# Optimization experiments

Hardware: AMD Instinct MI355X
Metric: run time of the kernel (lower is better)

The kernel has to match this reference:

```python
import jax, jax.numpy as jnp
import numpy as np

C = 1.0            # curvature
N = 50000          # nodes
E = 800000         # edges (avg degree 16)
D_IN = 127         # raw feature dim (+1 time col -> 128)
D = 128            # hidden dim
N_CLS = 40         # classes
EPS = 1e-8


def setup_inputs() -> dict:
    key = jax.random.key(0)
    ks = jax.random.split(key, 8)
    stdv = 1.0 / np.sqrt(D)
    node_feat = jax.random.normal(ks[0], (N, D_IN), jnp.float32)
    W1 = jax.random.uniform(ks[1], (D, D), jnp.float32, -stdv, stdv)
    W2 = jax.random.uniform(ks[2], (D, D), jnp.float32, -stdv, stdv)
    b1 = jnp.zeros((D,), jnp.float32)
    b2 = jnp.zeros((D,), jnp.float32)
    s1 = jnp.asarray(np.log(10.0), jnp.float32)
    s2 = jnp.asarray(np.log(10.0), jnp.float32)
    # class prototypes: random points on the hyperboloid <p,p>_L = -C
    cls_space = jax.random.normal(ks[3], (N_CLS, D - 1), jnp.float32) * stdv
    cls_time = jnp.sqrt(C + jnp.sum(cls_space * cls_space, -1, keepdims=True))
    cls = jnp.concatenate([cls_time, cls_space], axis=-1)
    cls_bias = jnp.zeros((N_CLS,), jnp.float32)
    edge_w = jax.random.uniform(ks[4], (E,), jnp.float32)
    edge_row = jax.random.randint(ks[5], (E,), 0, N, jnp.int32)
    edge_col = jax.random.randint(ks[6], (E,), 0, N, jnp.int32)
    return dict(node_feat=node_feat, W1=W1, b1=b1, s1=s1, W2=W2, b2=b2, s2=s2,
                cls=cls, cls_bias=cls_bias, edge_w=edge_w,
                edge_row=edge_row, edge_col=edge_col)


def _expmap0(u):
    # u: [N, D-1] spatial tangent at origin; lift to hyperboloid (k = C)
    sc = jnp.sqrt(C)
    nrm = jnp.clip(jnp.linalg.norm(u, axis=-1, keepdims=True), EPS)
    time = sc * jnp.cosh(nrm / sc)
    space = sc * jnp.sinh(nrm / sc) * (u / nrm)
    return jnp.concatenate([time, space], axis=-1)


def _lorentz_linear(x, W, b, log_s, nonlin):
    if nonlin:
        x = jax.nn.relu(x)
    x = x @ W.T + b                                   # [N, D]
    xn = x[:, 1:]                                     # spatial part
    time = jax.nn.sigmoid(x[:, :1]) * jnp.minimum(jnp.exp(log_s), 10.0) \
           + (jnp.sqrt(C) + 0.5)
    sq = jnp.clip(jnp.sum(xn * xn, -1, keepdims=True), EPS)
    scale = (time * time - C) / sq
    return jnp.concatenate([time, xn * jnp.sqrt(jnp.clip(scale, EPS))], axis=-1)


def _lorentz_agg(x, edge_w, edge_row, edge_col):
    # spmm: support[i] = sum_{(i,j) in E} w_ij * x[j]
    msg = x[edge_col] * edge_w[:, None]               # [E, D]
    s = jax.ops.segment_sum(msg, edge_row, num_segments=N)
    # -<s,s>_L = s0^2 - sum_{i>0} si^2
    neg_inner = s[:, :1] * s[:, :1] - jnp.sum(s[:, 1:] * s[:, 1:], -1, keepdims=True)
    denom = jnp.sqrt(jnp.clip(jnp.abs(neg_inner), EPS)) / jnp.sqrt(C)
    return s / denom


def reference(node_feat, W1, b1, s1, W2, b2, s2, cls, cls_bias,
              edge_w, edge_row, edge_col):
    x = _expmap0(node_feat)                           # [N, 128] on hyperboloid
    # layer 1 (no nonlin)
    x = _lorentz_linear(x, W1, b1, s1, nonlin=False)
    x = _lorentz_agg(x, edge_w, edge_row, edge_col)
    # layer 2 (relu)
    x = _lorentz_linear(x, W2, b2, s2, nonlin=True)
    x = _lorentz_agg(x, edge_w, edge_row, edge_col)
    # Lorentz decoder: 2c + 2*cinner(x, cls) + bias
    x_signed = jnp.concatenate([-x[:, :1], x[:, 1:]], axis=-1)
    logits = 2.0 * C + 2.0 * (x_signed @ cls.T) + cls_bias
    return logits
```

## Files before the change

kernel.cpp:

```cpp
#include <hip/hip_runtime.h>
#include <hip/hip_fp16.h>
#include <math.h>

#define NN 50000
#define DD 128
#define NCLS 40
#define EPSV 1e-8f
#define ELLCAP 64

typedef unsigned int uint4n __attribute__((ext_vector_type(4)));

__device__ __forceinline__ float waveReduceSum(float v) {
    for (int off = 32; off > 0; off >>= 1) v += __shfl_xor(v, off, 64);
    return v;
}

__device__ __forceinline__ float bcastlane0(float v) {
    return __int_as_float(__builtin_amdgcn_readfirstlane(__float_as_int(v)));
}

__device__ __forceinline__ float h_lo(unsigned int w) {
    return __half2float(__ushort_as_half((unsigned short)(w & 0xffffu)));
}
__device__ __forceinline__ float h_hi(unsigned int w) {
    return __half2float(__ushort_as_half((unsigned short)(w >> 16)));
}
__device__ __forceinline__ unsigned int h_pack(float a, float b) {
    return (unsigned int)__half_as_ushort(__float2half(a)) |
           ((unsigned int)__half_as_ushort(__float2half(b)) << 16);
}
__device__ __forceinline__ float fexp(float x) {
    return __builtin_amdgcn_exp2f(x * 1.44269504089f);
}
__device__ __forceinline__ float frcp(float x) { return __builtin_amdgcn_rcpf(x); }
__device__ __forceinline__ float frsq(float x) { return __builtin_amdgcn_rsqf(x); }


__global__ void fill_ell_kernel(const int* __restrict__ erow, const int* __restrict__ ecol,
                                const float* __restrict__ ew, int* __restrict__ cnt,
                                unsigned int* __restrict__ ell, int E) {
    for (int e = blockIdx.x * blockDim.x + threadIdx.x; e < E; e += gridDim.x * blockDim.x) {
        int r = erow[e];
        int p = atomicAdd(&cnt[r], 1);
        if (p < ELLCAP) {
            unsigned int packed = (unsigned int)ecol[e] |
                ((unsigned int)__half_as_ushort(__float2half(ew[e])) << 16);
            ell[(long)r * ELLCAP + p] = packed;
        }
    }
}

__global__ void packwt_kernel(const float* __restrict__ W1, unsigned int* __restrict__ p1,
                              const float* __restrict__ W2, unsigned int* __restrict__ p2) {
    int b = blockIdx.x;
    const float* W = (b < 32) ? W1 : W2;
    unsigned int* P = (b < 32) ? p1 : p2;
    int a = (b & 31) * 256 + threadIdx.x;
    int pr = a >> 7;
    int rem = a & 127;
    int l = rem >> 1, kl = rem & 1;
    int k = 2 * pr + kl;
    P[a] = h_pack(W[(2 * l) * 128 + k], W[(2 * l + 1) * 128 + k]);
}

#define RPW 8
__global__ __launch_bounds__(512, 4) void linear1_kernel(
    const float* __restrict__ X, const unsigned int* __restrict__ Wp,
    const float* __restrict__ bias, const float* __restrict__ logs,
    unsigned int* __restrict__ outh, int n)
{
    __shared__ unsigned int wS[8192];
    __shared__ float xrow[8][RPW * 128];
    int tid = threadIdx.x;
    int wid = tid >> 6, lane = tid & 63;
    #pragma unroll
    for (int i = 0; i < 4; ++i) {
        int idx = tid * 4 + i * 2048;
        *(uint4n*)(wS + idx) = *(const uint4n*)(Wp + idx);
    }
    __syncthreads();
    float2 bv = *(const float2*)(bias + 2 * lane);
    float sval = fminf(fexp(logs[0]), 10.f);
    float* xbase = xrow[wid];
    int nslabs = n / RPW;
    for (int slab = blockIdx.x * 8 + wid; slab < nslabs; slab += gridDim.x * 8) {
        int row0 = slab * RPW;
        #pragma unroll
        for (int r = 0; r < RPW; ++r) {
            int row = row0 + r;
            const float* src = X + (long)row * 127;
            float u0 = src[2 * lane];
            float u1 = (2 * lane + 1 < 127) ? src[2 * lane + 1] : 0.f;
            float ss = waveReduceSum(u0 * u0 + u1 * u1);
            float nrm = fmaxf(sqrtf(ss), EPSV);
            float ex = fexp(nrm), exn = fexp(-nrm);
            float ch = 0.5f * (ex + exn);
            float coef = 0.5f * (ex - exn) * frcp(nrm);
            if (lane == 0) xbase[r * 128] = ch;
            xbase[r * 128 + 1 + 2 * lane] = coef * u0;
            if (2 * lane + 1 < 127) xbase[r * 128 + 2 + 2 * lane] = coef * u1;
        }
        float2 acc[RPW];
        #pragma unroll
        for (int r = 0; r < RPW; ++r) acc[r] = make_float2(0.f, 0.f);
        #pragma unroll 4
        for (int k0 = 0; k0 < 128; k0 += 4) {
            uint2 wa = *(const uint2*)(wS + (k0 >> 1) * 128 + 2 * lane);
            uint2 wb = *(const uint2*)(wS + (k0 >> 1) * 128 + 128 + 2 * lane);
            float2 w0 = make_float2(h_lo(wa.x), h_hi(wa.x));
            float2 w1 = make_float2(h_lo(wa.y), h_hi(wa.y));
            float2 w2 = make_float2(h_lo(wb.x), h_hi(wb.x));
            float2 w3 = make_float2(h_lo(wb.y), h_hi(wb.y));
            #pragma unroll
            for (int r = 0; r < RPW; ++r) {
                float4 xq = *(const float4*)(xbase + r * 128 + k0);
                acc[r].x = fmaf(xq.x, w0.x, acc[r].x);
                acc[r].y = fmaf(xq.x, w0.y, acc[r].y);
                acc[r].x = fmaf(xq.y, w1.x, acc[r].x);
                acc[r].y = fmaf(xq.y, w1.y, acc[r].y);
                acc[r].x = fmaf(xq.z, w2.x, acc[r].x);
                acc[r].y = fmaf(xq.z, w2.y, acc[r].y);
                acc[r].x = fmaf(xq.w, w3.x, acc[r].x);
                acc[r].y = fmaf(xq.w, w3.y, acc[r].y);
            }
        }
        #pragma unroll
        for (int r = 0; r < RPW; ++r) {
            float ax = acc[r].x + bv.x;
            float ay = acc[r].y + bv.y;
            float t0 = __shfl(ax, 0, 64);
            float ssq = waveReduceSum(ax * ax + ay * ay);
            float timev = sval * frcp(1.f + fexp(-t0)) + 1.5f;
            float sq = fmaxf(ssq - t0 * t0, EPSV);
            float fac = sqrtf(fmaxf((timev * timev - 1.f) * frcp(sq), EPSV));
            float o0 = (lane == 0) ? timev : ax * fac;
            __builtin_nontemporal_store(h_pack(o0, ay * fac),
                                        &outh[(long)(row0 + r) * 64 + lane]);
        }
    }
}

__global__ __launch_bounds__(512, 4) void linear2_kernel(
    const unsigned int* __restrict__ Xh, const unsigned int* __restrict__ Wp,
    const float* __restrict__ bias, const float* __restrict__ logs,
    unsigned int* __restrict__ outh, int n)
{
    __shared__ unsigned int wS[8192];
    __shared__ float xrow[8][RPW * 128];
    int tid = threadIdx.x;
    int wid = tid >> 6, lane = tid & 63;
    #pragma unroll
    for (int i = 0; i < 4; ++i) {
        int idx = tid * 4 + i * 2048;
        *(uint4n*)(wS + idx) = *(const uint4n*)(Wp + idx);
    }
    __syncthreads();
    float2 bv = *(const float2*)(bias + 2 * lane);
    float sval = fminf(fexp(logs[0]), 10.f);
    float* xbase = xrow[wid];
    int nslabs = n / RPW;
    for (int slab = blockIdx.x * 8 + wid; slab < nslabs; slab += gridDim.x * 8) {
        int row0 = slab * RPW;
        #pragma unroll
        for (int r = 0; r < RPW; ++r) {
            unsigned int u = __builtin_nontemporal_load(&Xh[(long)(row0 + r) * 64 + lane]);
            *(float2*)(xbase + r * 128 + 2 * lane) = make_float2(h_lo(u), h_hi(u));
        }
        float2 acc[RPW];
        #pragma unroll
        for (int r = 0; r < RPW; ++r) acc[r] = make_float2(0.f, 0.f);
        #pragma unroll 4
        for (int k0 = 0; k0 < 128; k0 += 4) {
            uint2 wa = *(const uint2*)(wS + (k0 >> 1) * 128 + 2 * lane);
            uint2 wb = *(const uint2*)(wS + (k0 >> 1) * 128 + 128 + 2 * lane);
            float2 w0 = make_float2(h_lo(wa.x), h_hi(wa.x));
            float2 w1 = make_float2(h_lo(wa.y), h_hi(wa.y));
            float2 w2 = make_float2(h_lo(wb.x), h_hi(wb.x));
            float2 w3 = make_float2(h_lo(wb.y), h_hi(wb.y));
            #pragma unroll
            for (int r = 0; r < RPW; ++r) {
                float4 xq = *(const float4*)(xbase + r * 128 + k0);
                acc[r].x = fmaf(xq.x, w0.x, acc[r].x);
                acc[r].y = fmaf(xq.x, w0.y, acc[r].y);
                acc[r].x = fmaf(xq.y, w1.x, acc[r].x);
                acc[r].y = fmaf(xq.y, w1.y, acc[r].y);
                acc[r].x = fmaf(xq.z, w2.x, acc[r].x);
                acc[r].y = fmaf(xq.z, w2.y, acc[r].y);
                acc[r].x = fmaf(xq.w, w3.x, acc[r].x);
                acc[r].y = fmaf(xq.w, w3.y, acc[r].y);
            }
        }
        #pragma unroll
        for (int r = 0; r < RPW; ++r) {
            float ax = acc[r].x + bv.x;
            float ay = acc[r].y + bv.y;
            float t0 = __shfl(ax, 0, 64);
            float ssq = waveReduceSum(ax * ax + ay * ay);
            float timev = sval * frcp(1.f + fexp(-t0)) + 1.5f;
            float sq = fmaxf(ssq - t0 * t0, EPSV);
            float fac = sqrtf(fmaxf((timev * timev - 1.f) * frcp(sq), EPSV));
            float o0 = (lane == 0) ? timev : ax * fac;
            __builtin_nontemporal_store(h_pack(o0, ay * fac),
                                        &outh[(long)(row0 + r) * 64 + lane]);
        }
    }
}


#define GATHER_BODY(accs, eptr, idx)                                       \
    {                                                                      \
        unsigned int cw = eptr[idx];                                       \
        float w = h_hi(cw);                                                \
        uint4 xw = *(const uint4*)(Xh + (long)(cw & 0xffffu) * 64 + l16 * 4); \
        accs[0] = fmaf(w, h_lo(xw.x), accs[0]);                            \
        accs[1] = fmaf(w, h_hi(xw.x), accs[1]);                            \
        accs[2] = fmaf(w, h_lo(xw.y), accs[2]);                            \
        accs[3] = fmaf(w, h_hi(xw.y), accs[3]);                            \
        accs[4] = fmaf(w, h_lo(xw.z), accs[4]);                            \
        accs[5] = fmaf(w, h_hi(xw.z), accs[5]);                            \
        accs[6] = fmaf(w, h_lo(xw.w), accs[6]);                            \
        accs[7] = fmaf(w, h_hi(xw.w), accs[7]);                            \
    }

#define REDUCE8(accs)                                                      \
    _Pragma("unroll")                                                      \
    for (int q = 0; q < 8; ++q) {                                          \
        accs[q] += __shfl_xor(accs[q], 16, 64);                            \
        accs[q] += __shfl_xor(accs[q], 32, 64);                            \
    }

#define GATHER_PAIR()                                                      \
    int rowA = 2 * pair, rowB = rowA + 1;                                  \
    int cA = min(cnt[rowA], ELLCAP), cB = min(cnt[rowB], ELLCAP);          \
    const unsigned int* eA = ell + (long)rowA * ELLCAP;                    \
    const unsigned int* eB = ell + (long)rowB * ELLCAP;                    \
    float aA[8] = {0,0,0,0,0,0,0,0};                                       \
    float aB[8] = {0,0,0,0,0,0,0,0};                                       \
    {                                                                      \
        int ia = g, ib = g;                                                \
        while (ia < cA && ib < cB) {                                       \
            GATHER_BODY(aA, eA, ia)                                        \
            GATHER_BODY(aB, eB, ib)                                        \
            ia += 4; ib += 4;                                              \
        }                                                                  \
        while (ia < cA) { GATHER_BODY(aA, eA, ia) ia += 4; }               \
        while (ib < cB) { GATHER_BODY(aB, eB, ib) ib += 4; }               \
    }                                                                      \
    REDUCE8(aA)                                                            \
    REDUCE8(aB)

#define SS16(ss)                                                           \
    ss += __shfl_xor(ss, 1, 64); ss += __shfl_xor(ss, 2, 64);              \
    ss += __shfl_xor(ss, 4, 64); ss += __shfl_xor(ss, 8, 64);

__global__ __launch_bounds__(256, 8) void gather_norm_kernel(
    const unsigned int* __restrict__ Xh, const int* __restrict__ cnt,
    const unsigned int* __restrict__ ell, unsigned int* __restrict__ outh, int n)
{
    int wid = threadIdx.x >> 6, lane = threadIdx.x & 63;
    int g = lane >> 4, l16 = lane & 15;
    int npairs = n >> 1;
    for (int pair = blockIdx.x * 4 + wid; pair < npairs; pair += gridDim.x * 4) {
        GATHER_PAIR()
        float ssA = aA[0]*aA[0]+aA[1]*aA[1]+aA[2]*aA[2]+aA[3]*aA[3]
                  + aA[4]*aA[4]+aA[5]*aA[5]+aA[6]*aA[6]+aA[7]*aA[7];
        float ssB = aB[0]*aB[0]+aB[1]*aB[1]+aB[2]*aB[2]+aB[3]*aB[3]
                  + aB[4]*aB[4]+aB[5]*aB[5]+aB[6]*aB[6]+aB[7]*aB[7];
        SS16(ssA)
        SS16(ssB)
        float t0A = bcastlane0(aA[0]);
        float t0B = bcastlane0(aB[0]);
        float invA = frsq(fmaxf(fabsf(2.f * t0A * t0A - ssA), EPSV));
        float invB = frsq(fmaxf(fabsf(2.f * t0B * t0B - ssB), EPSV));
        if (g == 0) {
            uint4n o;
            o.x = h_pack(fmaxf(aA[0]*invA,0.f), fmaxf(aA[1]*invA,0.f));
            o.y = h_pack(fmaxf(aA[2]*invA,0.f), fmaxf(aA[3]*invA,0.f));
            o.z = h_pack(fmaxf(aA[4]*invA,0.f), fmaxf(aA[5]*invA,0.f));
            o.w = h_pack(fmaxf(aA[6]*invA,0.f), fmaxf(aA[7]*invA,0.f));
            __builtin_nontemporal_store(o, (uint4n*)(outh + (long)rowA * 64 + l16 * 4));
        } else if (g == 1) {
            uint4n o;
            o.x = h_pack(fmaxf(aB[0]*invB,0.f), fmaxf(aB[1]*invB,0.f));
            o.y = h_pack(fmaxf(aB[2]*invB,0.f), fmaxf(aB[3]*invB,0.f));
            o.z = h_pack(fmaxf(aB[4]*invB,0.f), fmaxf(aB[5]*invB,0.f));
            o.w = h_pack(fmaxf(aB[6]*invB,0.f), fmaxf(aB[7]*invB,0.f));
            __builtin_nontemporal_store(o, (uint4n*)(outh + (long)rowB * 64 + l16 * 4));
        }
    }
}

__global__ __launch_bounds__(256, 8) void gather_logits_kernel(
    const unsigned int* __restrict__ Xh, const int* __restrict__ cnt,
    const unsigned int* __restrict__ ell,
    const float* __restrict__ cls, const float* __restrict__ cbias,
    float* __restrict__ outp, int n)
{
    __shared__ unsigned int clsP[NCLS * 66];
    __shared__ float cbS[NCLS];
    __shared__ float xsrow[4][2][128];
    int tid = threadIdx.x;
    for (int idx = tid; idx < NCLS * 64; idx += 256) {
        int c = idx >> 6, kk = idx & 63;
        clsP[c * 66 + kk] = h_pack(cls[c * 128 + 2 * kk], cls[c * 128 + 2 * kk + 1]);
    }
    if (tid < NCLS) cbS[tid] = cbias[tid];
    __syncthreads();
    int wid = tid >> 6, lane = tid & 63;
    int g = lane >> 4, l16 = lane & 15;
    float* xsA = xsrow[wid][0];
    float* xsB = xsrow[wid][1];
    int npairs = n >> 1;
    for (int pair = blockIdx.x * 4 + wid; pair < npairs; pair += gridDim.x * 4) {
        GATHER_PAIR()
        float ssA = aA[0]*aA[0]+aA[1]*aA[1]+aA[2]*aA[2]+aA[3]*aA[3]
                  + aA[4]*aA[4]+aA[5]*aA[5]+aA[6]*aA[6]+aA[7]*aA[7];
        float ssB = aB[0]*aB[0]+aB[1]*aB[1]+aB[2]*aB[2]+aB[3]*aB[3]
                  + aB[4]*aB[4]+aB[5]*aB[5]+aB[6]*aB[6]+aB[7]*aB[7];
        SS16(ssA)
        SS16(ssB)
        float t0A = bcastlane0(aA[0]);
        float t0B = bcastlane0(aB[0]);
        float invA = frsq(fmaxf(fabsf(2.f * t0A * t0A - ssA), EPSV));
        float invB = frsq(fmaxf(fabsf(2.f * t0B * t0B - ssB), EPSV));
        if (g == 0) {
            float v0 = aA[0] * invA;
            if (l16 == 0) v0 = -v0;
            float* xp = xsA + l16 * 8;
            *(float4*)xp       = make_float4(v0, aA[1]*invA, aA[2]*invA, aA[3]*invA);
            *(float4*)(xp + 4) = make_float4(aA[4]*invA, aA[5]*invA, aA[6]*invA, aA[7]*invA);
        } else if (g == 1) {
            float v0 = aB[0] * invB;
            if (l16 == 0) v0 = -v0;
            float* xp = xsB + l16 * 8;
            *(float4*)xp       = make_float4(v0, aB[1]*invB, aB[2]*invB, aB[3]*invB);
            *(float4*)(xp + 4) = make_float4(aB[4]*invB, aB[5]*invB, aB[6]*invB, aB[7]*invB);
        }
        if (lane < NCLS) {
            float dA = 0.f, dB = 0.f;
            const unsigned int* cp = clsP + lane * 66;
            #pragma unroll 8
            for (int kk = 0; kk < 64; ++kk) {
                unsigned int u = cp[kk];
                float c0 = h_lo(u), c1 = h_hi(u);
                float2 xa = *(const float2*)(xsA + 2 * kk);
                float2 xb = *(const float2*)(xsB + 2 * kk);
                dA = fmaf(c0, xa.x, dA); dA = fmaf(c1, xa.y, dA);
                dB = fmaf(c0, xb.x, dB); dB = fmaf(c1, xb.y, dB);
            }
            outp[(long)rowA * NCLS + lane] = 2.f + 2.f * dA + cbS[lane];
            outp[(long)rowB * NCLS + lane] = 2.f + 2.f * dB + cbS[lane];
        }
    }
}


extern "C" void kernel_launch(void* const* d_in, const int* in_sizes, int n_in,
                              void* d_out, int out_size, void* d_ws, size_t ws_size,
                              hipStream_t stream) {
    const float* node_feat = (const float*)d_in[0];
    const float* W1   = (const float*)d_in[1];
    const float* b1   = (const float*)d_in[2];
    const float* s1   = (const float*)d_in[3];
    const float* W2   = (const float*)d_in[4];
    const float* b2   = (const float*)d_in[5];
    const float* s2   = (const float*)d_in[6];
    const float* cls  = (const float*)d_in[7];
    const float* cb   = (const float*)d_in[8];
    const float* ew   = (const float*)d_in[9];
    const int*   erow = (const int*)d_in[10];
    const int*   ecol = (const int*)d_in[11];
    float* outp = (float*)d_out;

    const int n = NN;
    const int E = in_sizes[9];

    unsigned int* bufH1 = (unsigned int*)d_ws;
    unsigned int* bufH2 = bufH1 + (size_t)NN * 64;
    int*   cnt    = (int*)(bufH2 + (size_t)NN * 64);
    unsigned int* ell = (unsigned int*)(cnt + NN);
    unsigned int* wp1 = ell + (size_t)NN * ELLCAP;
    unsigned int* wp2 = wp1 + 128 * 64;

    (void)hipMemsetAsync(cnt, 0, (size_t)NN * sizeof(int), stream);
    packwt_kernel<<<64, 256, 0, stream>>>(W1, wp1, W2, wp2);
    fill_ell_kernel<<<2048, 256, 0, stream>>>(erow, ecol, ew, cnt, ell, E);

    const int LGRID = (n / RPW + 7) / 8;
    const int PGRID = ((n >> 1) + 3) / 4;

    linear1_kernel<<<LGRID, 512, 0, stream>>>(node_feat, wp1, b1, s1, bufH1, n);
    gather_norm_kernel<<<PGRID, 256, 0, stream>>>(bufH1, cnt, ell, bufH2, n);
    linear2_kernel<<<LGRID, 512, 0, stream>>>(bufH2, wp2, b2, s2, bufH1, n);
    gather_logits_kernel<<<PGRID, 256, 0, stream>>>(bufH1, cnt, ell, cls, cb, outp, n);
}
```

Measured before the change: 230.2 us.

## Use packed fp16 dot2 instructions in linear kernels with half-precision shared rows

Both Lorentz linear kernels now keep activation rows in shared memory as packed fp16 pairs and compute the matmul with v_dot2 fp16 instructions. This replaces the per-element half-to-float conversions and scalar FMAs, and the weight packing layout is changed to pair consecutive k values. In linear1, the expmap output is divided by cosh before packing to fp16 to avoid overflow, and the accumulator is rescaled by cosh afterwards. This halves shared memory traffic for the activations and roughly halves ALU instructions, at the cost of fp16 rounding on the activations.

```diff
diff --git a/kernel.cpp b/kernel.cpp
--- a/kernel.cpp
+++ b/kernel.cpp
@@ -9,6 +9,28 @@
 #define ELLCAP 64
 
 typedef unsigned int uint4n __attribute__((ext_vector_type(4)));
+typedef _Float16 h2 __attribute__((ext_vector_type(2)));
+
+__device__ __forceinline__ float h_lo(unsigned int w) {
+    return __half2float(__ushort_as_half((unsigned short)(w & 0xffffu)));
+}
+__device__ __forceinline__ float h_hi(unsigned int w) {
+    return __half2float(__ushort_as_half((unsigned short)(w >> 16)));
+}
+
+__device__ __forceinline__ h2 as_h2(unsigned int u) {
+    union { unsigned int i; h2 h; } c; c.i = u; return c.h;
+}
+
+#if __has_builtin(__builtin_amdgcn_fdot2)
+#define FDOT2(xu, wu, acc) acc = __builtin_amdgcn_fdot2(as_h2(xu), as_h2(wu), acc, false);
+#else
+#define FDOT2(xu, wu, acc)                                                  \
+    {                                                                       \
+        acc = fmaf(h_lo(xu), h_lo(wu), acc);                                \
+        acc = fmaf(h_hi(xu), h_hi(wu), acc);                                \
+    }
+#endif
 
 __device__ __forceinline__ float waveReduceSum(float v) {
     for (int off = 32; off > 0; off >>= 1) v += __shfl_xor(v, off, 64);
@@ -19,12 +41,6 @@
     return __int_as_float(__builtin_amdgcn_readfirstlane(__float_as_int(v)));
 }
 
-__device__ __forceinline__ float h_lo(unsigned int w) {
-    return __half2float(__ushort_as_half((unsigned short)(w & 0xffffu)));
-}
-__device__ __forceinline__ float h_hi(unsigned int w) {
-    return __half2float(__ushort_as_half((unsigned short)(w >> 16)));
-}
 __device__ __forceinline__ unsigned int h_pack(float a, float b) {
     return (unsigned int)__half_as_ushort(__float2half(a)) |
            ((unsigned int)__half_as_ushort(__float2half(b)) << 16);
@@ -56,11 +72,8 @@
     const float* W = (b < 32) ? W1 : W2;
     unsigned int* P = (b < 32) ? p1 : p2;
     int a = (b & 31) * 256 + threadIdx.x;
-    int pr = a >> 7;
-    int rem = a & 127;
-    int l = rem >> 1, kl = rem & 1;
-    int k = 2 * pr + kl;
-    P[a] = h_pack(W[(2 * l) * 128 + k], W[(2 * l + 1) * 128 + k]);
+    int kk = a >> 7, col = a & 127;
+    P[a] = h_pack(W[col * 128 + 2 * kk], W[col * 128 + 2 * kk + 1]);
 }
 
 #define RPW 8
@@ -70,7 +83,7 @@
     unsigned int* __restrict__ outh, int n)
 {
     __shared__ unsigned int wS[8192];
-    __shared__ float xrow[8][RPW * 128];
+    __shared__ unsigned int xS[8][RPW * 64];
     int tid = threadIdx.x;
     int wid = tid >> 6, lane = tid & 63;
     #pragma unroll
@@ -81,10 +94,11 @@
     __syncthreads();
     float2 bv = *(const float2*)(bias + 2 * lane);
     float sval = fminf(fexp(logs[0]), 10.f);
-    float* xbase = xrow[wid];
+    unsigned int* xbase = xS[wid];
     int nslabs = n / RPW;
     for (int slab = blockIdx.x * 8 + wid; slab < nslabs; slab += gridDim.x * 8) {
         int row0 = slab * RPW;
+        float chv[RPW];
         #pragma unroll
         for (int r = 0; r < RPW; ++r) {
             int row = row0 + r;
@@ -96,38 +110,34 @@
             float ex = fexp(nrm), exn = fexp(-nrm);
             float ch = 0.5f * (ex + exn);
             float coef = 0.5f * (ex - exn) * frcp(nrm);
-            if (lane == 0) xbase[r * 128] = ch;
-            xbase[r * 128 + 1 + 2 * lane] = coef * u0;
-            if (2 * lane + 1 < 127) xbase[r * 128 + 2 + 2 * lane] = coef * u1;
+            chv[r] = ch;
+            float inv_ch = frcp(ch);
+            float u1p = __shfl(u1, (lane + 63) & 63, 64);
+            float xa = (lane == 0) ? 1.f : coef * u1p * inv_ch;
+            xbase[r * 64 + lane] = h_pack(xa, coef * u0 * inv_ch);
         }
         float2 acc[RPW];
         #pragma unroll
         for (int r = 0; r < RPW; ++r) acc[r] = make_float2(0.f, 0.f);
         #pragma unroll 4
-        for (int k0 = 0; k0 < 128; k0 += 4) {
-            uint2 wa = *(const uint2*)(wS + (k0 >> 1) * 128 + 2 * lane);
-            uint2 wb = *(const uint2*)(wS + (k0 >> 1) * 128 + 128 + 2 * lane);
-            float2 w0 = make_float2(h_lo(wa.x), h_hi(wa.x));
-            float2 w1 = make_float2(h_lo(wa.y), h_hi(wa.y));
-            float2 w2 = make_float2(h_lo(wb.x), h_hi(wb.x));
-            float2 w3 = make_float2(h_lo(wb.y), h_hi(wb.y));
+        for (int kk0 = 0; kk0 < 64; kk0 += 4) {
+            uint2 wp0 = *(const uint2*)(wS + (kk0 + 0) * 128 + 2 * lane);
+            uint2 wp1 = *(const uint2*)(wS + (kk0 + 1) * 128 + 2 * lane);
+            uint2 wp2 = *(const uint2*)(wS + (kk0 + 2) * 128 + 2 * lane);
+            uint2 wp3 = *(const uint2*)(wS + (kk0 + 3) * 128 + 2 * lane);
             #pragma unroll
             for (int r = 0; r < RPW; ++r) {
-                float4 xq = *(const float4*)(xbase + r * 128 + k0);
-                acc[r].x = fmaf(xq.x, w0.x, acc[r].x);
-                acc[r].y = fmaf(xq.x, w0.y, acc[r].y);
-                acc[r].x = fmaf(xq.y, w1.x, acc[r].x);
-                acc[r].y = fmaf(xq.y, w1.y, acc[r].y);
-                acc[r].x = fmaf(xq.z, w2.x, acc[r].x);
-                acc[r].y = fmaf(xq.z, w2.y, acc[r].y);
-                acc[r].x = fmaf(xq.w, w3.x, acc[r].x);
-                acc[r].y = fmaf(xq.w, w3.y, acc[r].y);
+                uint4 xq = *(const uint4*)(xbase + r * 64 + kk0);
+                FDOT2(xq.x, wp0.x, acc[r].x) FDOT2(xq.x, wp0.y, acc[r].y)
+                FDOT2(xq.y, wp1.x, acc[r].x) FDOT2(xq.y, wp1.y, acc[r].y)
+                FDOT2(xq.z, wp2.x, acc[r].x) FDOT2(xq.z, wp2.y, acc[r].y)
+                FDOT2(xq.w, wp3.x, acc[r].x) FDOT2(xq.w, wp3.y, acc[r].y)
             }
         }
         #pragma unroll
         for (int r = 0; r < RPW; ++r) {
-            float ax = acc[r].x + bv.x;
-            float ay = acc[r].y + bv.y;
+            float ax = acc[r].x * chv[r] + bv.x;
+            float ay = acc[r].y * chv[r] + bv.y;
             float t0 = __shfl(ax, 0, 64);
             float ssq = waveReduceSum(ax * ax + ay * ay);
             float timev = sval * frcp(1.f + fexp(-t0)) + 1.5f;
@@ -146,7 +156,7 @@
     unsigned int* __restrict__ outh, int n)
 {
     __shared__ unsigned int wS[8192];
-    __shared__ float xrow[8][RPW * 128];
+    __shared__ unsigned int xS[8][RPW * 64];
     int tid = threadIdx.x;
     int wid = tid >> 6, lane = tid & 63;
     #pragma unroll
@@ -157,37 +167,30 @@
     __syncthreads();
     float2 bv = *(const float2*)(bias + 2 * lane);
     float sval = fminf(fexp(logs[0]), 10.f);
-    float* xbase = xrow[wid];
+    unsigned int* xbase = xS[wid];
     int nslabs = n / RPW;
     for (int slab = blockIdx.x * 8 + wid; slab < nslabs; slab += gridDim.x * 8) {
         int row0 = slab * RPW;
         #pragma unroll
-        for (int r = 0; r < RPW; ++r) {
-            unsigned int u = __builtin_nontemporal_load(&Xh[(long)(row0 + r) * 64 + lane]);
-            *(float2*)(xbase + r * 128 + 2 * lane) = make_float2(h_lo(u), h_hi(u));
-        }
+        for (int r = 0; r < RPW; ++r)
+            xbase[r * 64 + lane] =
+                __builtin_nontemporal_load(&Xh[(long)(row0 + r) * 64 + lane]);
         float2 acc[RPW];
         #pragma unroll
         for (int r = 0; r < RPW; ++r) acc[r] = make_float2(0.f, 0.f);
         #pragma unroll 4
-        for (int k0 = 0; k0 < 128; k0 += 4) {
-            uint2 wa = *(const uint2*)(wS + (k0 >> 1) * 128 + 2 * lane);
-            uint2 wb = *(const uint2*)(wS + (k0 >> 1) * 128 + 128 + 2 * lane);
-            float2 w0 = make_float2(h_lo(wa.x), h_hi(wa.x));
-            float2 w1 = make_float2(h_lo(wa.y), h_hi(wa.y));
-            float2 w2 = make_float2(h_lo(wb.x), h_hi(wb.x));
-            float2 w3 = make_float2(h_lo(wb.y), h_hi(wb.y));
+        for (int kk0 = 0; kk0 < 64; kk0 += 4) {
+            uint2 wp0 = *(const uint2*)(wS + (kk0 + 0) * 128 + 2 * lane);
+            uint2 wp1 = *(const uint2*)(wS + (kk0 + 1) * 128 + 2 * lane);
+            uint2 wp2 = *(const uint2*)(wS + (kk0 + 2) * 128 + 2 * lane);
+            uint2 wp3 = *(const uint2*)(wS + (kk0 + 3) * 128 + 2 * lane);
             #pragma unroll
             for (int r = 0; r < RPW; ++r) {
-                float4 xq = *(const float4*)(xbase + r * 128 + k0);
-                acc[r].x = fmaf(xq.x, w0.x, acc[r].x);
-                acc[r].y = fmaf(xq.x, w0.y, acc[r].y);
-                acc[r].x = fmaf(xq.y, w1.x, acc[r].x);
-                acc[r].y = fmaf(xq.y, w1.y, acc[r].y);
-                acc[r].x = fmaf(xq.z, w2.x, acc[r].x);
-                acc[r].y = fmaf(xq.z, w2.y, acc[r].y);
-                acc[r].x = fmaf(xq.w, w3.x, acc[r].x);
-                acc[r].y = fmaf(xq.w, w3.y, acc[r].y);
+                uint4 xq = *(const uint4*)(xbase + r * 64 + kk0);
+                FDOT2(xq.x, wp0.x, acc[r].x) FDOT2(xq.x, wp0.y, acc[r].y)
+                FDOT2(xq.y, wp1.x, acc[r].x) FDOT2(xq.y, wp1.y, acc[r].y)
+                FDOT2(xq.z, wp2.x, acc[r].x) FDOT2(xq.z, wp2.y, acc[r].y)
+                FDOT2(xq.w, wp3.x, acc[r].x) FDOT2(xq.w, wp3.y, acc[r].y)
             }
         }
         #pragma unroll
```

Result: faster. 217.3 us (-5.6%).
